# Performance work log

Measured on AMD Instinct MI355X. Metric: run time of the kernel, lower is better.

The kernel has to match this reference:

```python
import jax, jax.numpy as jnp
import numpy as np

NEG_INF = -1e9  # mask fill value used by the original module


def setup_inputs() -> dict:
    key = jax.random.key(0)
    k1, k2, k3 = jax.random.split(key, 3)
    B, S, D, DQK = 4, 4096, 1024, 64
    encodings = jax.random.normal(k1, (B, S, D), dtype=jnp.float32)
    # nn.Linear weight layout: [out_features, in_features]
    W_q = jax.random.normal(k2, (DQK, D), dtype=jnp.float32) * (1.0 / np.sqrt(D))
    W_k = jax.random.normal(k3, (DQK, D), dtype=jnp.float32) * (1.0 / np.sqrt(D))
    return {"encodings": encodings, "W_q": W_q, "W_k": W_k}


def reference(encodings, W_q, W_k):
    # q, k: [B, S, d_qk]
    q = jnp.einsum('bsd,ed->bse', encodings, W_q)
    k = jnp.einsum('bsd,ed->bse', encodings, W_k)
    d_qk = k.shape[-1]
    # scores: [B, S, S]
    sims = jnp.einsum('bqe,bke->bqk', q, k) / jnp.sqrt(jnp.float32(d_qk))
    S = encodings.shape[1]
    # causal mask: mask strictly-upper triangle (future positions)
    causal = jnp.triu(jnp.ones((S, S), dtype=bool), k=1)
    sims = jnp.where(causal[None, :, :], jnp.float32(NEG_INF), sims)
    attn = jax.nn.softmax(sims, axis=-1)
    # values are the raw encodings (no W_v in this module)
    return jnp.einsum('bqk,bkd->bqd', attn, encodings)
```

## Files before the change

### kernel.cpp

```cpp
#include <hip/hip_runtime.h>

typedef __bf16 bf16;
typedef bf16 bf16x8 __attribute__((ext_vector_type(8)));
typedef float f32x4 __attribute__((ext_vector_type(4)));
typedef unsigned int u32;
typedef unsigned short u16;

#define BB 4
#define SS 4096
#define DD 1024
#define EE 64
static constexpr float SCALE2 = 0.18033688011112042f;
static constexpr float MFIX = 16.0f;

#define MFMA(a,b,c) __builtin_amdgcn_mfma_f32_16x16x32_bf16((a),(b),(c),0,0,0)

typedef __attribute__((address_space(3))) unsigned int lds_u32;
typedef const __attribute__((address_space(1))) unsigned int glb_u32;

static __device__ __forceinline__ void gload16(const void* g, void* l) {
    __builtin_amdgcn_global_load_lds((glb_u32*)g, (lds_u32*)l, 16, 0, 0);
}

static __device__ __forceinline__ u16 f2bf(float x) {
    union { float f; u32 u; } v; v.f = x;
    u32 r = v.u + 0x7FFFu + ((v.u >> 16) & 1u);
    return (u16)(r >> 16);
}
static __device__ __forceinline__ u32 pk2(float a, float b) {
    return (u32)f2bf(a) | ((u32)f2bf(b) << 16);
}
static __device__ __forceinline__ float fexp2(float x) {
    return __builtin_amdgcn_exp2f(x);
}

__global__ __launch_bounds__(512, 4) void k_prep(const float* __restrict__ enc,
                                                 const float* __restrict__ wq,
                                                 const float* __restrict__ wk,
                                                 u16* __restrict__ qout,
                                                 u16* __restrict__ kout,
                                                 u16* __restrict__ vt) {
    __shared__ __align__(16) u16 sm[12288];
    const int tid = threadIdx.x;
    if (blockIdx.x < 256) {
        u16* la = sm;
        u16* lw = sm + 4096;
        const int m0 = blockIdx.x * 64;
        const int w = tid >> 6, lane = tid & 63, l15 = lane & 15, quad = lane >> 4;
        const int ari = tid >> 3, ag = tid & 7;
        const int wri = tid >> 2, wg = (tid & 3) * 2;
        const float* arow = enc + (size_t)(m0 + ari) * DD + ag * 8;
        const float* wrow = ((wri < 64) ? (wq + (size_t)wri * DD) : (wk + (size_t)(wri - 64) * DD)) + (tid & 3) * 16;

        float4 a0 = *(const float4*)(arow);
        float4 a1 = *(const float4*)(arow + 4);
        float4 b0 = *(const float4*)(wrow);
        float4 b1 = *(const float4*)(wrow + 4);
        float4 b2 = *(const float4*)(wrow + 8);
        float4 b3 = *(const float4*)(wrow + 12);

        f32x4 acc[4];
#pragma unroll
        for (int i = 0; i < 4; i++) acc[i] = f32x4{0.f, 0.f, 0.f, 0.f};

        for (int kk = 0; kk < DD; kk += 64) {
            uint4 pa, pw0, pw1;
            pa.x = pk2(a0.x, a0.y); pa.y = pk2(a0.z, a0.w);
            pa.z = pk2(a1.x, a1.y); pa.w = pk2(a1.z, a1.w);
            pw0.x = pk2(b0.x, b0.y); pw0.y = pk2(b0.z, b0.w);
            pw0.z = pk2(b1.x, b1.y); pw0.w = pk2(b1.z, b1.w);
            pw1.x = pk2(b2.x, b2.y); pw1.y = pk2(b2.z, b2.w);
            pw1.z = pk2(b3.x, b3.y); pw1.w = pk2(b3.z, b3.w);
            __syncthreads();
            *(uint4*)&la[ari * 64 + (ag ^ (ari & 7)) * 8] = pa;
            *(uint4*)&lw[wri * 64 + ((wg + 0) ^ (wri & 7)) * 8] = pw0;
            *(uint4*)&lw[wri * 64 + ((wg + 1) ^ (wri & 7)) * 8] = pw1;
            __syncthreads();
            if (kk + 64 < DD) {
                a0 = *(const float4*)(arow + kk + 64);
                a1 = *(const float4*)(arow + kk + 68);
                b0 = *(const float4*)(wrow + kk + 64);
                b1 = *(const float4*)(wrow + kk + 68);
                b2 = *(const float4*)(wrow + kk + 72);
                b3 = *(const float4*)(wrow + kk + 76);
            }
            int m = 16 * (w & 3) + l15;
#pragma unroll
            for (int es = 0; es < 2; es++) {
                bf16x8 af = *(const bf16x8*)&la[m * 64 + ((((es << 2) + quad) ^ (m & 7))) * 8];
#pragma unroll
                for (int ct = 0; ct < 4; ct++) {
                    int n = 64 * (w >> 2) + 16 * ct + l15;
                    bf16x8 bf_ = *(const bf16x8*)&lw[n * 64 + ((((es << 2) + quad) ^ (n & 7))) * 8];
                    acc[ct] = MFMA(af, bf_, acc[ct]);
                }
            }
        }
#pragma unroll
        for (int ct = 0; ct < 4; ct++) {
            int n = 64 * (w >> 2) + 16 * ct + l15;
            u16* dst = (n < 64) ? qout : kout;
            int col = n & 63;
#pragma unroll
            for (int r = 0; r < 4; r++) {
                int grow = m0 + 16 * (w & 3) + 4 * quad + r;
                dst[(size_t)grow * EE + col] = f2bf(acc[ct][r]);
            }
        }
    } else {
        u32* lt2 = (u32*)sm + (tid >> 8) * 2144;
        const int t = tid & 255;
        const int tc = blockIdx.x - 256;
        const int dt = tc & 15, stp = (tc >> 4) & 31, b = tc >> 9;
        const int st = stp * 2 + (tid >> 8);
        const int srow = t >> 2, d0 = (t & 3) << 4;
        const float* src = enc + ((size_t)(b * SS + st * 64 + srow) * DD) + dt * 64 + d0;
        float4 f0 = ((const float4*)src)[0];
        float4 f1 = ((const float4*)src)[1];
        float4 f2 = ((const float4*)src)[2];
        float4 f3 = ((const float4*)src)[3];
        float v[16];
        v[0] = f0.x; v[1] = f0.y; v[2] = f0.z; v[3] = f0.w;
        v[4] = f1.x; v[5] = f1.y; v[6] = f1.z; v[7] = f1.w;
        v[8] = f2.x; v[9] = f2.y; v[10] = f2.z; v[11] = f2.w;
        v[12] = f3.x; v[13] = f3.y; v[14] = f3.z; v[15] = f3.w;
#pragma unroll
        for (int j = 0; j < 8; j++) lt2[((d0 >> 1) + j) * 67 + srow] = pk2(v[2 * j], v[2 * j + 1]);
        __syncthreads();
        const int dp = t >> 3, soct = t & 7;
        u32 a[8];
#pragma unroll
        for (int j = 0; j < 8; j++) a[j] = lt2[dp * 67 + soct * 8 + j];
        uint4 r0, r1;
        r0.x = (a[0] & 0xffffu) | (a[1] << 16);
        r0.y = (a[2] & 0xffffu) | (a[3] << 16);
        r0.z = (a[4] & 0xffffu) | (a[5] << 16);
        r0.w = (a[6] & 0xffffu) | (a[7] << 16);
        r1.x = (a[0] >> 16) | (a[1] & 0xffff0000u);
        r1.y = (a[2] >> 16) | (a[3] & 0xffff0000u);
        r1.z = (a[4] >> 16) | (a[5] & 0xffff0000u);
        r1.w = (a[6] >> 16) | (a[7] & 0xffff0000u);
        u16* dst0 = vt + ((size_t)(b * DD + dt * 64 + 2 * dp) * SS) + st * 64 + soct * 8;
        *(uint4*)dst0 = r0;
        *(uint4*)(dst0 + SS) = r1;
    }
}

__global__ __launch_bounds__(512, 2) void k_attn(const u16* __restrict__ qg, const u16* __restrict__ kg,
                                                 const u16* __restrict__ vt, float* __restrict__ out) {
    __shared__ __align__(16) u16 lds[49408];
    u16* lp = lds;
    float* lsum = (float*)&lds[8192];
    const int tid = threadIdx.x;
    const int w = tid >> 6, lane = tid & 63, l15 = lane & 15, quad = lane >> 4;
    const int pr = blockIdx.x & 15, combo = blockIdx.x >> 4;
    const int ds = combo & 3, b = combo >> 2;
    const int d0 = ds * 256;
    const int kr = w & 1, qc = w >> 1;
    const int dc = w & 3, qr = w >> 2;
    const u16* kbase = kg + (size_t)b * SS * EE;
    const u16* vbase = vt + ((size_t)b * DD + d0) * SS;

    const int kgrow = tid >> 3, kglog = (tid & 7) ^ (kgrow & 7);
    const u16* kptr = kbase + (size_t)kgrow * EE + kglog * 8;
    const u16* vptr0; const u16* vptr1; const u16* vptr2; const u16* vptr3;
    {
        int go0 = 0 * 512 + tid, gr0 = go0 >> 3, gl0 = (go0 & 7) ^ (gr0 & 7);
        int go1 = 1 * 512 + tid, gr1 = go1 >> 3, gl1 = (go1 & 7) ^ (gr1 & 7);
        int go2 = 2 * 512 + tid, gr2 = go2 >> 3, gl2 = (go2 & 7) ^ (gr2 & 7);
        int go3 = 3 * 512 + tid, gr3 = go3 >> 3, gl3 = (go3 & 7) ^ (gr3 & 7);
        vptr0 = vbase + (size_t)gr0 * SS + gl0 * 8;
        vptr1 = vbase + (size_t)gr1 * SS + gl1 * 8;
        vptr2 = vbase + (size_t)gr2 * SS + gl2 * 8;
        vptr3 = vbase + (size_t)gr3 * SS + gl3 * 8;
    }

    for (int half = 0; half < 2; half++) {
        const int qt = half ? pr : (31 - pr);
        const int q0 = qt * 128;
        const int KT = 2 * qt + 2;
        const u16* qbase = qg + ((size_t)b * SS + q0) * EE;
        __syncthreads();
        if (tid < 128) lsum[tid] = 0.f;
        {
            int goff = tid, grow = goff >> 3, glog = (goff & 7) ^ (grow & 7);
            gload16(kbase + (size_t)grow * EE + glog * 8, (void*)&lds[8448 + goff * 8]);
#pragma unroll
            for (int i = 0; i < 4; i++) {
                int go = i * 512 + tid, gr = go >> 3, gl = (go & 7) ^ (gr & 7);
                gload16(vbase + (size_t)gr * SS + gl * 8, (void*)&lds[8448 + 4096 + go * 8]);
            }
        }
        bf16x8 qf[2][2];
#pragma unroll
        for (int ct = 0; ct < 2; ct++) {
            int qv = 32 * qc + 16 * ct + l15;
#pragma unroll
            for (int es = 0; es < 2; es++)
                qf[ct][es] = *(const bf16x8*)(qbase + (size_t)qv * EE + es * 32 + quad * 8);
        }
        f32x4 o[4][4];
#pragma unroll
        for (int i = 0; i < 4; i++)
#pragma unroll
            for (int j = 0; j < 4; j++) o[i][j] = f32x4{0.f, 0.f, 0.f, 0.f};
        float rl[2] = {0.f, 0.f};
        __syncthreads();

        for (int kt = 0; kt < KT; kt++) {
            const int k0 = kt * 64;
            const u16* lk = &lds[8448 + (kt & 1) * 20480];
            const u16* lv = lk + 4096;
            const bool dg = (kt >= KT - 2);
            const bool pf = (kt + 1 < KT);
            uint4 gk, gv0, gv1, gv2, gv3;
            if (pf) {
                const int k1 = k0 + 64;
                gk  = *(const uint4*)(kptr + (size_t)k1 * EE);
                gv0 = *(const uint4*)(vptr0 + k1);
                gv1 = *(const uint4*)(vptr1 + k1);
                gv2 = *(const uint4*)(vptr2 + k1);
                gv3 = *(const uint4*)(vptr3 + k1);
            }
#pragma unroll
            for (int rt = 0; rt < 2; rt++) {
                int m = 32 * kr + 16 * rt + l15;
                bf16x8 ka0 = *(const bf16x8*)&lk[m * 64 + ((quad ^ (m & 7))) * 8];
                bf16x8 ka1 = *(const bf16x8*)&lk[m * 64 + (((4 + quad) ^ (m & 7))) * 8];
#pragma unroll
                for (int ct = 0; ct < 2; ct++) {
                    f32x4 c = f32x4{0.f, 0.f, 0.f, 0.f};
                    c = MFMA(ka0, qf[ct][0], c);
                    c = MFMA(ka1, qf[ct][1], c);
                    int qv = 32 * qc + 16 * ct + l15;
                    float p[4];
#pragma unroll
                    for (int r = 0; r < 4; r++) {
                        float arg = __builtin_fmaf(c[r], SCALE2, -MFIX);
                        if (dg) {
                            int kp = k0 + 32 * kr + 16 * rt + 4 * quad + r;
                            if (kp > q0 + qv) arg = -3.0e38f;
                        }
                        p[r] = fexp2(arg);
                    }
                    rl[ct] += (p[0] + p[1]) + (p[2] + p[3]);
                    int g16 = 4 * kr + 2 * rt + (quad >> 1);
                    uint2 pkk;
                    pkk.x = pk2(p[0], p[1]);
                    pkk.y = pk2(p[2], p[3]);
                    *(uint2*)&lp[qv * 64 + (g16 ^ (qv & 7)) * 8 + (quad & 1) * 4] = pkk;
                }
            }
            __syncthreads();
            if (pf) {
                u16* nb = &lds[8448 + ((kt + 1) & 1) * 20480];
                *(uint4*)&nb[tid * 8] = gk;
                *(uint4*)&nb[4096 + (0 * 512 + tid) * 8] = gv0;
                *(uint4*)&nb[4096 + (1 * 512 + tid) * 8] = gv1;
                *(uint4*)&nb[4096 + (2 * 512 + tid) * 8] = gv2;
                *(uint4*)&nb[4096 + (3 * 512 + tid) * 8] = gv3;
            }
#pragma unroll
            for (int ks = 0; ks < 2; ks++) {
                bf16x8 vb[4];
#pragma unroll
                for (int ct = 0; ct < 4; ct++) {
                    int n = 64 * dc + 16 * ct + l15;
                    vb[ct] = *(const bf16x8*)&lv[n * 64 + ((((ks << 2) + quad) ^ (n & 7))) * 8];
                }
#pragma unroll
                for (int rt = 0; rt < 4; rt++) {
                    int m = 64 * qr + 16 * rt + l15;
                    bf16x8 pa = *(const bf16x8*)&lp[m * 64 + ((((ks << 2) + quad) ^ (m & 7))) * 8];
#pragma unroll
                    for (int ct = 0; ct < 4; ct++) o[rt][ct] = MFMA(pa, vb[ct], o[rt][ct]);
                }
            }
            __syncthreads();
        }
#pragma unroll
        for (int ct = 0; ct < 2; ct++) {
            float t = rl[ct];
            t += __shfl_xor(t, 16, 64);
            t += __shfl_xor(t, 32, 64);
            if (quad == 0) atomicAdd(&lsum[32 * qc + 16 * ct + l15], t);
        }
        __syncthreads();
        float* obase = out + ((size_t)b * SS + q0) * DD + d0 + dc * 64;
#pragma unroll
        for (int rt = 0; rt < 4; rt++) {
#pragma unroll
            for (int r = 0; r < 4; r++) {
                int row = 64 * qr + 16 * rt + 4 * quad + r;
                float li = 1.0f / lsum[row];
#pragma unroll
                for (int ct = 0; ct < 4; ct++)
                    obase[(size_t)row * DD + ct * 16 + l15] = o[rt][ct][r] * li;
            }
        }
    }
}

extern "C" void kernel_launch(void* const* d_in, const int* in_sizes, int n_in,
                              void* d_out, int out_size, void* d_ws, size_t ws_size,
                              hipStream_t stream) {
    (void)in_sizes; (void)n_in; (void)out_size; (void)ws_size;
    const float* enc = (const float*)d_in[0];
    const float* wq = (const float*)d_in[1];
    const float* wk = (const float*)d_in[2];
    char* ws = (char*)d_ws;
    u16* qbf = (u16*)ws;
    u16* kbf = (u16*)(ws + (2ull << 20));
    u16* vt  = (u16*)(ws + (4ull << 20));
    float* out = (float*)d_out;

    hipLaunchKernelGGL(k_prep, dim3(2304), dim3(512), 0, stream, enc, wq, wk, qbf, kbf, vt);
    hipLaunchKernelGGL(k_attn, dim3(256), dim3(512), 0, stream, qbf, kbf, vt, out);
}
```

Measured before the change: 244.0 us.

## Software-pipeline QK^T/softmax with PV across tiles using double-buffered P and K

Restructures the attention loop into a skewed pipeline: at step p it computes scores and probabilities for tile p while running the PV MFMAs for tile p-1. The P buffer, K buffer and V buffer are double-buffered, which cuts the barriers per iteration from two to one. K prefetch now goes directly to LDS via global_load_lds, and bf16 packing uses native conversions instead of manual rounding. This raises LDS usage, which may affect occupancy, and adds one extra loop step per half.

```diff
diff --git a/kernel.cpp b/kernel.cpp
--- a/kernel.cpp
+++ b/kernel.cpp
@@ -1,6 +1,7 @@
 #include <hip/hip_runtime.h>
 
 typedef __bf16 bf16;
+typedef bf16 bf16x2 __attribute__((ext_vector_type(2)));
 typedef bf16 bf16x8 __attribute__((ext_vector_type(8)));
 typedef float f32x4 __attribute__((ext_vector_type(4)));
 typedef unsigned int u32;
@@ -23,12 +24,12 @@
 }
 
 static __device__ __forceinline__ u16 f2bf(float x) {
-    union { float f; u32 u; } v; v.f = x;
-    u32 r = v.u + 0x7FFFu + ((v.u >> 16) & 1u);
-    return (u16)(r >> 16);
+    union { bf16 h; u16 u; } v; v.h = (bf16)x;
+    return v.u;
 }
 static __device__ __forceinline__ u32 pk2(float a, float b) {
-    return (u32)f2bf(a) | ((u32)f2bf(b) << 16);
+    bf16x2 t; t[0] = (bf16)a; t[1] = (bf16)b;
+    return __builtin_bit_cast(u32, t);
 }
 static __device__ __forceinline__ float fexp2(float x) {
     return __builtin_amdgcn_exp2f(x);
@@ -148,9 +149,8 @@
 
 __global__ __launch_bounds__(512, 2) void k_attn(const u16* __restrict__ qg, const u16* __restrict__ kg,
                                                  const u16* __restrict__ vt, float* __restrict__ out) {
-    __shared__ __align__(16) u16 lds[49408];
-    u16* lp = lds;
-    float* lsum = (float*)&lds[8192];
+    __shared__ __align__(16) u16 lds[57600];
+    float* lsum = (float*)&lds[16384];
     const int tid = threadIdx.x;
     const int w = tid >> 6, lane = tid & 63, l15 = lane & 15, quad = lane >> 4;
     const int pr = blockIdx.x & 15, combo = blockIdx.x >> 4;
@@ -163,7 +163,7 @@
 
     const int kgrow = tid >> 3, kglog = (tid & 7) ^ (kgrow & 7);
     const u16* kptr = kbase + (size_t)kgrow * EE + kglog * 8;
-    const u16* vptr0; const u16* vptr1; const u16* vptr2; const u16* vptr3;
+    const u16 *vptr0, *vptr1, *vptr2, *vptr3;
     {
         int go0 = 0 * 512 + tid, gr0 = go0 >> 3, gl0 = (go0 & 7) ^ (gr0 & 7);
         int go1 = 1 * 512 + tid, gr1 = go1 >> 3, gl1 = (go1 & 7) ^ (gr1 & 7);
@@ -182,15 +182,11 @@
         const u16* qbase = qg + ((size_t)b * SS + q0) * EE;
         __syncthreads();
         if (tid < 128) lsum[tid] = 0.f;
-        {
-            int goff = tid, grow = goff >> 3, glog = (goff & 7) ^ (grow & 7);
-            gload16(kbase + (size_t)grow * EE + glog * 8, (void*)&lds[8448 + goff * 8]);
-#pragma unroll
-            for (int i = 0; i < 4; i++) {
-                int go = i * 512 + tid, gr = go >> 3, gl = (go & 7) ^ (gr & 7);
-                gload16(vbase + (size_t)gr * SS + gl * 8, (void*)&lds[8448 + 4096 + go * 8]);
-            }
-        }
+        gload16(kptr, (void*)&lds[16640 + tid * 8]);
+        gload16(vptr0, (void*)&lds[24832 + (0 * 512 + tid) * 8]);
+        gload16(vptr1, (void*)&lds[24832 + (1 * 512 + tid) * 8]);
+        gload16(vptr2, (void*)&lds[24832 + (2 * 512 + tid) * 8]);
+        gload16(vptr3, (void*)&lds[24832 + (3 * 512 + tid) * 8]);
         bf16x8 qf[2][2];
 #pragma unroll
         for (int ct = 0; ct < 2; ct++) {
@@ -205,75 +201,78 @@
 #pragma unroll
             for (int j = 0; j < 4; j++) o[i][j] = f32x4{0.f, 0.f, 0.f, 0.f};
         float rl[2] = {0.f, 0.f};
+        uint4 gv0, gv1, gv2, gv3;
         __syncthreads();
 
-        for (int kt = 0; kt < KT; kt++) {
-            const int k0 = kt * 64;
-            const u16* lk = &lds[8448 + (kt & 1) * 20480];
-            const u16* lv = lk + 4096;
-            const bool dg = (kt >= KT - 2);
-            const bool pf = (kt + 1 < KT);
-            uint4 gk, gv0, gv1, gv2, gv3;
-            if (pf) {
-                const int k1 = k0 + 64;
-                gk  = *(const uint4*)(kptr + (size_t)k1 * EE);
+        for (int p = 0; p <= KT; p++) {
+            if (p >= 1 && p < KT) {
+                u16* nv = &lds[24832 + (p & 1) * 16384];
+                *(uint4*)&nv[(0 * 512 + tid) * 8] = gv0;
+                *(uint4*)&nv[(1 * 512 + tid) * 8] = gv1;
+                *(uint4*)&nv[(2 * 512 + tid) * 8] = gv2;
+                *(uint4*)&nv[(3 * 512 + tid) * 8] = gv3;
+            }
+            if (p + 1 < KT) {
+                const int k1 = (p + 1) * 64;
+                gload16(kptr + (size_t)k1 * EE, (void*)&lds[16640 + ((p + 1) & 1) * 4096 + tid * 8]);
                 gv0 = *(const uint4*)(vptr0 + k1);
                 gv1 = *(const uint4*)(vptr1 + k1);
                 gv2 = *(const uint4*)(vptr2 + k1);
                 gv3 = *(const uint4*)(vptr3 + k1);
             }
-#pragma unroll
-            for (int rt = 0; rt < 2; rt++) {
-                int m = 32 * kr + 16 * rt + l15;
-                bf16x8 ka0 = *(const bf16x8*)&lk[m * 64 + ((quad ^ (m & 7))) * 8];
-                bf16x8 ka1 = *(const bf16x8*)&lk[m * 64 + (((4 + quad) ^ (m & 7))) * 8];
-#pragma unroll
-                for (int ct = 0; ct < 2; ct++) {
-                    f32x4 c = f32x4{0.f, 0.f, 0.f, 0.f};
-                    c = MFMA(ka0, qf[ct][0], c);
-                    c = MFMA(ka1, qf[ct][1], c);
-                    int qv = 32 * qc + 16 * ct + l15;
-                    float p[4];
-#pragma unroll
-                    for (int r = 0; r < 4; r++) {
-                        float arg = __builtin_fmaf(c[r], SCALE2, -MFIX);
-                        if (dg) {
-                            int kp = k0 + 32 * kr + 16 * rt + 4 * quad + r;
-                            if (kp > q0 + qv) arg = -3.0e38f;
+            if (p < KT) {
+                const int k0 = p * 64;
+                const u16* lk = &lds[16640 + (p & 1) * 4096];
+                u16* lpw = &lds[(p & 1) * 8192];
+                const bool dg = (p >= KT - 2);
+#pragma unroll
+                for (int rt = 0; rt < 2; rt++) {
+                    int m = 32 * kr + 16 * rt + l15;
+                    bf16x8 ka0 = *(const bf16x8*)&lk[m * 64 + ((quad ^ (m & 7))) * 8];
+                    bf16x8 ka1 = *(const bf16x8*)&lk[m * 64 + (((4 + quad) ^ (m & 7))) * 8];
+#pragma unroll
+                    for (int ct = 0; ct < 2; ct++) {
+                        f32x4 c = f32x4{0.f, 0.f, 0.f, 0.f};
+                        c = MFMA(ka0, qf[ct][0], c);
+                        c = MFMA(ka1, qf[ct][1], c);
+                        int qv = 32 * qc + 16 * ct + l15;
+                        float pv[4];
+#pragma unroll
+                        for (int r = 0; r < 4; r++) {
+                            float arg = __builtin_fmaf(c[r], SCALE2, -MFIX);
+                            if (dg) {
+                                int kp = k0 + 32 * kr + 16 * rt + 4 * quad + r;
+                                if (kp > q0 + qv) arg = -3.0e38f;
+                            }
+                            pv[r] = fexp2(arg);
                         }
-                        p[r] = fexp2(arg);
+                        rl[ct] += (pv[0] + pv[1]) + (pv[2] + pv[3]);
+                        int g16 = 4 * kr + 2 * rt + (quad >> 1);
+                        uint2 pkk;
+                        pkk.x = pk2(pv[0], pv[1]);
+                        pkk.y = pk2(pv[2], pv[3]);
+                        *(uint2*)&lpw[qv * 64 + (g16 ^ (qv & 7)) * 8 + (quad & 1) * 4] = pkk;
                     }
-                    rl[ct] += (p[0] + p[1]) + (p[2] + p[3]);
-                    int g16 = 4 * kr + 2 * rt + (quad >> 1);
-                    uint2 pkk;
-                    pkk.x = pk2(p[0], p[1]);
-                    pkk.y = pk2(p[2], p[3]);
-                    *(uint2*)&lp[qv * 64 + (g16 ^ (qv & 7)) * 8 + (quad & 1) * 4] = pkk;
                 }
             }
-            __syncthreads();
-            if (pf) {
-                u16* nb = &lds[8448 + ((kt + 1) & 1) * 20480];
-                *(uint4*)&nb[tid * 8] = gk;
-                *(uint4*)&nb[4096 + (0 * 512 + tid) * 8] = gv0;
-                *(uint4*)&nb[4096 + (1 * 512 + tid) * 8] = gv1;
-                *(uint4*)&nb[4096 + (2 * 512 + tid) * 8] = gv2;
-                *(uint4*)&nb[4096 + (3 * 512 + tid) * 8] = gv3;
-            }
-#pragma unroll
-            for (int ks = 0; ks < 2; ks++) {
-                bf16x8 vb[4];
-#pragma unroll
-                for (int ct = 0; ct < 4; ct++) {
-                    int n = 64 * dc + 16 * ct + l15;
-                    vb[ct] = *(const bf16x8*)&lv[n * 64 + ((((ks << 2) + quad) ^ (n & 7))) * 8];
-                }
-#pragma unroll
-                for (int rt = 0; rt < 4; rt++) {
-                    int m = 64 * qr + 16 * rt + l15;
-                    bf16x8 pa = *(const bf16x8*)&lp[m * 64 + ((((ks << 2) + quad) ^ (m & 7))) * 8];
-#pragma unroll
-                    for (int ct = 0; ct < 4; ct++) o[rt][ct] = MFMA(pa, vb[ct], o[rt][ct]);
+            if (p >= 1) {
+                const u16* lv = &lds[24832 + ((p - 1) & 1) * 16384];
+                const u16* lpr = &lds[((p - 1) & 1) * 8192];
+#pragma unroll
+                for (int ks = 0; ks < 2; ks++) {
+                    bf16x8 vb[4];
+#pragma unroll
+                    for (int ct = 0; ct < 4; ct++) {
+                        int n = 64 * dc + 16 * ct + l15;
+                        vb[ct] = *(const bf16x8*)&lv[n * 64 + ((((ks << 2) + quad) ^ (n & 7))) * 8];
+                    }
+#pragma unroll
+                    for (int rt = 0; rt < 4; rt++) {
+                        int m = 64 * qr + 16 * rt + l15;
+                        bf16x8 pa = *(const bf16x8*)&lpr[m * 64 + ((((ks << 2) + quad) ^ (m & 7))) * 8];
+#pragma unroll
+                        for (int ct = 0; ct < 4; ct++) o[rt][ct] = MFMA(pa, vb[ct], o[rt][ct]);
+                    }
                 }
             }
             __syncthreads();
```

New measurement: 236.8 us. 1.03x faster.
